# Kernel tuning notes

Hardware: AMD Instinct MI355X
Metric: run time of the kernel (lower is better)

The kernel has to match this reference:

```python
import jax, jax.numpy as jnp
import numpy as np

HIDDEN = 1024
NUM_HEADS = 16
HEAD_DIM = HIDDEN // NUM_HEADS  # 64
B, S = 2, 2048


def setup_inputs() -> dict:
    key = jax.random.key(0)
    ks = jax.random.split(key, 10)
    sd = 1.0 / np.sqrt(HIDDEN)
    x = jax.random.normal(ks[0], (B, S, HIDDEN), dtype=jnp.float32)
    # per-head projections stacked over head axis: [H, hidden, head_dim]
    Wq = jax.random.normal(ks[1], (NUM_HEADS, HIDDEN, HEAD_DIM), dtype=jnp.float32) * sd
    Wk = jax.random.normal(ks[2], (NUM_HEADS, HIDDEN, HEAD_DIM), dtype=jnp.float32) * sd
    Wv = jax.random.normal(ks[3], (NUM_HEADS, HIDDEN, HEAD_DIM), dtype=jnp.float32) * sd
    bq = jax.random.normal(ks[4], (NUM_HEADS, HEAD_DIM), dtype=jnp.float32) * sd
    bk = jax.random.normal(ks[5], (NUM_HEADS, HEAD_DIM), dtype=jnp.float32) * sd
    bv = jax.random.normal(ks[6], (NUM_HEADS, HEAD_DIM), dtype=jnp.float32) * sd
    # output projection: [all_head_size, hidden]
    Wo = jax.random.normal(ks[7], (HIDDEN, HIDDEN), dtype=jnp.float32) * sd
    bo = jax.random.normal(ks[8], (HIDDEN,), dtype=jnp.float32) * sd
    return {"x": x, "Wq": Wq, "bq": bq, "Wk": Wk, "bk": bk,
            "Wv": Wv, "bv": bv, "Wo": Wo, "bo": bo}


def reference(x, Wq, bq, Wk, bk, Wv, bv, Wo, bo):
    # Fused-across-heads equivalent of the per-head Python loop.
    # q,k,v: [B, H, S, Dh]
    q = jnp.einsum('bsd,hde->bhse', x, Wq) + bq[None, :, None, :]
    k = jnp.einsum('bsd,hde->bhse', x, Wk) + bk[None, :, None, :]
    v = jnp.einsum('bsd,hde->bhse', x, Wv) + bv[None, :, None, :]
    scale = 1.0 / jnp.sqrt(jnp.asarray(HEAD_DIM, dtype=x.dtype))
    scores = jnp.einsum('bhse,bhte->bhst', q, k) * scale  # [B,H,S,S]
    probs = jax.nn.softmax(scores, axis=-1)               # dropout=0 (eval)
    ctx = jnp.einsum('bhst,bhte->bhse', probs, v)         # [B,H,S,Dh]
    # concat heads on last dim (head order matches torch.cat over heads)
    ctx = jnp.transpose(ctx, (0, 2, 1, 3)).reshape(x.shape[0], x.shape[1], -1)
    out = ctx @ Wo + bo                                   # output projection
    return out
```

## Files before the change

### kernel.cpp

```cpp
#include <hip/hip_runtime.h>
#include <cstdint>

typedef unsigned short u16;
typedef __attribute__((ext_vector_type(8))) short short8;
typedef __attribute__((ext_vector_type(4))) short short4v;
typedef __attribute__((ext_vector_type(4))) float f32x4;
typedef __attribute__((ext_vector_type(4))) unsigned short u16x4;

__device__ __forceinline__ u16 f2bf(float x) {
    unsigned int u = __float_as_uint(x);
    u += 0x7fffu + ((u >> 16) & 1u);
    return (u16)(u >> 16);
}

__device__ __forceinline__ float fexp2(float x) {
#if __has_builtin(__builtin_amdgcn_exp2f)
    return __builtin_amdgcn_exp2f(x);
#else
    return exp2f(x);
#endif
}

__device__ __forceinline__ unsigned pack_bf16(float a, float b) {
    unsigned ua = __float_as_uint(a) + 0x8000u;
    unsigned ub = __float_as_uint(b) + 0x8000u;
    return __builtin_amdgcn_perm(ub, ua, 0x07060302u);
}

#if __has_builtin(__builtin_amdgcn_mfma_f32_16x16x16bf16_1k)
__device__ __forceinline__ f32x4 mfma16(short4v a, short4v b, f32x4 c) {
    return __builtin_amdgcn_mfma_f32_16x16x16bf16_1k(a, b, c, 0, 0, 0);
}
#else
__device__ __forceinline__ f32x4 mfma16(short4v a, short4v b, f32x4 c) {
    short8 a8 = {a[0], a[1], a[2], a[3], 0, 0, 0, 0};
    short8 b8 = {b[0], b[1], b[2], b[3], 0, 0, 0, 0};
    return __builtin_amdgcn_mfma_f32_16x16x32_bf16(a8, b8, c, 0, 0, 0);
}
#endif

__device__ __forceinline__ void gload_lds16(const u16* g, u16* l) {
    __builtin_amdgcn_global_load_lds(
        (const __attribute__((address_space(1))) void*)(g),
        (__attribute__((address_space(3))) void*)(l),
        16, 0, 0);
}

__global__ __launch_bounds__(256) void cast_x_kernel(const float* __restrict__ x,
                                                     u16* __restrict__ xb) {
    int i = (blockIdx.x * 256 + threadIdx.x) * 4;
    float4 v = *(const float4*)(x + i);
    u16x4 o;
    o.x = f2bf(v.x); o.y = f2bf(v.y); o.z = f2bf(v.z); o.w = f2bf(v.w);
    *(u16x4*)(xb + i) = o;
}

__global__ __launch_bounds__(256) void transpose_cast_kernel(const float* __restrict__ src,
                                                             u16* __restrict__ dst,
                                                             int R, int C) {
    __shared__ u16 tile[64][65];
    const int rb = blockIdx.x * 64, cb = blockIdx.y * 64;
    const size_t matoff = (size_t)blockIdx.z * R * C;
    src += matoff; dst += matoff;
    const int tc = threadIdx.x & 63, tr = threadIdx.x >> 6;
    #pragma unroll
    for (int i = 0; i < 64; i += 4)
        tile[tr + i][tc] = f2bf(src[(size_t)(rb + tr + i) * C + (cb + tc)]);
    __syncthreads();
    #pragma unroll
    for (int i = 0; i < 64; i += 4)
        dst[(size_t)(cb + tr + i) * R + (rb + tc)] = tile[tc][tr + i];
}

__global__ __launch_bounds__(256) void gemm_qkv_kernel(
    const u16* __restrict__ X, const u16* __restrict__ W,
    const float* __restrict__ bq, const float* __restrict__ bk,
    const float* __restrict__ bv,
    u16* __restrict__ qo, u16* __restrict__ ko, u16* __restrict__ vto)
{
    __shared__ __align__(16) u16 As[128 * 32];
    __shared__ __align__(16) u16 Bs[128 * 32];
    const int tid = threadIdx.x;
    const int lane = tid & 63;
    const int wv = tid >> 6;
    const int wm = wv & 1, wn = wv >> 1;
    const int m0 = blockIdx.x * 128;
    const int n0 = blockIdx.y * 128;
    const int c = lane & 15, qd = lane >> 4;

    f32x4 acc[4][4];
    #pragma unroll
    for (int a = 0; a < 4; ++a)
        #pragma unroll
        for (int b2 = 0; b2 < 4; ++b2) acc[a][b2] = f32x4{0.f, 0.f, 0.f, 0.f};

    const u16* Xb = X + (size_t)m0 * 1024;
    const u16* Wb = W + (size_t)n0 * 1024;

    for (int kt = 0; kt < 1024; kt += 32) {
        #pragma unroll
        for (int i = 0; i < 2; ++i) {
            int slot = i * 256 + tid;
            int row = slot >> 2, part = slot & 3;
            gload_lds16(Xb + (size_t)row * 1024 + kt + part * 8, &As[slot * 8]);
            gload_lds16(Wb + (size_t)row * 1024 + kt + part * 8, &Bs[slot * 8]);
        }
        __syncthreads();
        short8 af[4], bf[4];
        #pragma unroll
        for (int mt = 0; mt < 4; ++mt)
            af[mt] = *(const short8*)&As[(wm * 64 + mt * 16 + c) * 32 + qd * 8];
        #pragma unroll
        for (int nt = 0; nt < 4; ++nt)
            bf[nt] = *(const short8*)&Bs[(wn * 64 + nt * 16 + c) * 32 + qd * 8];
        #pragma unroll
        for (int mt = 0; mt < 4; ++mt)
            #pragma unroll
            for (int nt = 0; nt < 4; ++nt)
                acc[mt][nt] = __builtin_amdgcn_mfma_f32_16x16x32_bf16(af[mt], bf[nt], acc[mt][nt], 0, 0, 0);
        __syncthreads();
    }

    #pragma unroll
    for (int mt = 0; mt < 4; ++mt) {
        const int mbase = m0 + wm * 64 + mt * 16 + qd * 4;
        const int b = mbase >> 11;
        #pragma unroll
        for (int nt = 0; nt < 4; ++nt) {
            const int n = n0 + wn * 64 + nt * 16 + c;
            const int mat = n >> 10;
            const int idx = n & 1023;
            const int h = idx >> 6, e = idx & 63;
            const float bias = (mat == 0 ? bq : (mat == 1 ? bk : bv))[idx];
            if (mat == 2) {
                const int s = mbase & 2047;
                u16x4 pv;
                pv.x = f2bf(acc[mt][nt][0] + bias);
                pv.y = f2bf(acc[mt][nt][1] + bias);
                pv.z = f2bf(acc[mt][nt][2] + bias);
                pv.w = f2bf(acc[mt][nt][3] + bias);
                *(u16x4*)(vto + ((((size_t)(b * 16 + h) * 128 + (s >> 4)) * 64 + e) * 16
                                 + (s & 15))) = pv;
            } else {
                const float scale = (mat == 0) ? 0.18033688011112042f : 1.0f;
                u16* dst = (mat == 0) ? qo : ko;
                #pragma unroll
                for (int r = 0; r < 4; ++r) {
                    const int s = (mbase + r) & 2047;
                    dst[((size_t)((b * 16 + h) * 2048 + s)) * 64 + e] =
                        f2bf((acc[mt][nt][r] + bias) * scale);
                }
            }
        }
    }
}

__global__ __launch_bounds__(256) void flash_kernel(
    const u16* __restrict__ Q,
    const u16* __restrict__ K,
    const u16* __restrict__ V2,
    u16* __restrict__ ctx)
{
    __shared__ __align__(16) char pool[34816];
    u16* stage = (u16*)pool;
    float (*Os)[64][66] = (float (*)[64][66])pool;
    float (*Ls)[64] = (float (*)[64])(pool + 33792);

    const int tid = threadIdx.x, lane = tid & 63, w = tid >> 6;
    const int c = lane & 15, qd = lane >> 4;
    const int bid = blockIdx.x;
    const int r5 = bid & 31;
    const int bh = (r5 & 7) * 4 + (r5 >> 3);
    const int q0 = (bid >> 5) * 64;
    const int b = bh >> 4, h = bh & 15;
    const u16* Qh = Q + (size_t)bh * 2048 * 64;
    const u16* Kh = K + (size_t)bh * 2048 * 64;
    const u16* Vh = V2 + (size_t)bh * 128 * 1024;

    u16* Kst = stage + w * 4096;
    u16* Vst = Kst + 2048;

    const int krow8 = lane >> 3;
    const int kgc = (lane & 7) ^ (krow8 & 7);

    short8 qf[4][2];
    #pragma unroll
    for (int qb = 0; qb < 4; ++qb)
        #pragma unroll
        for (int kb = 0; kb < 2; ++kb)
            qf[qb][kb] = *(const short8*)&Qh[(size_t)(q0 + qb * 16 + c) * 64 + kb * 32 + qd * 8];

    f32x4 o[4][4];
    f32x4 ol[4];
    #pragma unroll
    for (int mt = 0; mt < 4; ++mt)
        #pragma unroll
        for (int qb = 0; qb < 4; ++qb) o[mt][qb] = f32x4{0.f, 0.f, 0.f, 0.f};
    #pragma unroll
    for (int qb = 0; qb < 4; ++qb) ol[qb] = f32x4{0.f, 0.f, 0.f, 0.f};
    const short4v ones = {(short)0x3F80, (short)0x3F80, (short)0x3F80, (short)0x3F80};

    {
        const int t0 = w * 512;
        #pragma unroll
        for (int j = 0; j < 2; ++j) {
            const int row = j * 8 + krow8;
            gload_lds16(Kh + (size_t)(t0 + row) * 64 + kgc * 8, Kst + j * 512 + lane * 8);
            gload_lds16(Vh + (size_t)(w * 32) * 1024 + (j * 64 + lane) * 8,
                        Vst + j * 512 + lane * 8);
        }
    }

    for (int it = 0; it < 32; ++it) {
        const int buf = it & 1;
        u16* Kb = Kst + buf * 1024;
        u16* Vb = Vst + buf * 1024;

        __builtin_amdgcn_s_waitcnt(0);
        __builtin_amdgcn_sched_barrier(0);

        short8 kf[2];
        #pragma unroll
        for (int kb = 0; kb < 2; ++kb)
            kf[kb] = *(const short8*)&Kb[c * 64 + ((4 * kb + qd) ^ (c & 7)) * 8];
        short4v vf[4];
        #pragma unroll
        for (int mt = 0; mt < 4; ++mt)
            vf[mt] = *(const short4v*)&Vb[(mt * 16 + c) * 16 + qd * 4];

        __builtin_amdgcn_sched_barrier(0);

        if (it < 31) {
            const int t0n = w * 512 + (it + 1) * 16;
            u16* Kn = Kst + (buf ^ 1) * 1024;
            u16* Vn = Vst + (buf ^ 1) * 1024;
            #pragma unroll
            for (int j = 0; j < 2; ++j) {
                const int row = j * 8 + krow8;
                gload_lds16(Kh + (size_t)(t0n + row) * 64 + kgc * 8, Kn + j * 512 + lane * 8);
                gload_lds16(Vh + (size_t)(t0n >> 4) * 1024 + (j * 64 + lane) * 8,
                            Vn + j * 512 + lane * 8);
            }
        }

        f32x4 sc[4];
        #pragma unroll
        for (int qb = 0; qb < 4; ++qb) {
            sc[qb] = f32x4{0.f, 0.f, 0.f, 0.f};
            sc[qb] = __builtin_amdgcn_mfma_f32_16x16x32_bf16(kf[0], qf[qb][0], sc[qb], 0, 0, 0);
            sc[qb] = __builtin_amdgcn_mfma_f32_16x16x32_bf16(kf[1], qf[qb][1], sc[qb], 0, 0, 0);
        }

        short4v pb[4];
        #pragma unroll
        for (int qb = 0; qb < 4; ++qb) {
            float p0 = fexp2(sc[qb][0]);
            float p1 = fexp2(sc[qb][1]);
            float p2 = fexp2(sc[qb][2]);
            float p3 = fexp2(sc[qb][3]);
            unsigned d0 = pack_bf16(p0, p1);
            unsigned d1 = pack_bf16(p2, p3);
            union { unsigned u[2]; short4v s; } pu;
            pu.u[0] = d0; pu.u[1] = d1;
            pb[qb] = pu.s;
        }

        #pragma unroll
        for (int qb = 0; qb < 4; ++qb) {
            #pragma unroll
            for (int mt = 0; mt < 4; ++mt)
                o[mt][qb] = mfma16(vf[mt], pb[qb], o[mt][qb]);
            ol[qb] = mfma16(ones, pb[qb], ol[qb]);
        }
    }

    __syncthreads();
    if (qd == 0) {
        #pragma unroll
        for (int qb = 0; qb < 4; ++qb) Ls[w][qb * 16 + c] = ol[qb][0];
    }

    if (w >= 2) {
        float (*S)[66] = Os[w - 2];
        #pragma unroll
        for (int mt = 0; mt < 4; ++mt)
            #pragma unroll
            for (int qb = 0; qb < 4; ++qb)
                #pragma unroll
                for (int r = 0; r < 4; ++r)
                    S[mt * 16 + qd * 4 + r][qb * 16 + c] = o[mt][qb][r];
    }
    __syncthreads();
    if (w < 2) {
        float (*S)[66] = Os[w];
        #pragma unroll
        for (int mt = 0; mt < 4; ++mt)
            #pragma unroll
            for (int qb = 0; qb < 4; ++qb)
                #pragma unroll
                for (int r = 0; r < 4; ++r)
                    o[mt][qb][r] += S[mt * 16 + qd * 4 + r][qb * 16 + c];
    }
    __syncthreads();
    if (w == 1) {
        float (*S)[66] = Os[0];
        #pragma unroll
        for (int mt = 0; mt < 4; ++mt)
            #pragma unroll
            for (int qb = 0; qb < 4; ++qb)
                #pragma unroll
                for (int r = 0; r < 4; ++r)
                    S[mt * 16 + qd * 4 + r][qb * 16 + c] = o[mt][qb][r];
    }
    __syncthreads();
    if (w == 0) {
        float (*S)[66] = Os[0];
        float inv[4];
        #pragma unroll
        for (int qb = 0; qb < 4; ++qb) {
            int q = qb * 16 + c;
            float l = (Ls[0][q] + Ls[1][q]) + (Ls[2][q] + Ls[3][q]);
            inv[qb] = __builtin_amdgcn_rcpf(l);
        }
        #pragma unroll
        for (int mt = 0; mt < 4; ++mt)
            #pragma unroll
            for (int qb = 0; qb < 4; ++qb) {
                u16x4 ov;
                #pragma unroll
                for (int r = 0; r < 4; ++r) {
                    float v = (o[mt][qb][r] + S[mt * 16 + qd * 4 + r][qb * 16 + c]) * inv[qb];
                    ((u16*)&ov)[r] = f2bf(v);
                }
                *(u16x4*)&ctx[((size_t)(b * 2048 + q0 + qb * 16 + c)) * 1024
                              + h * 64 + mt * 16 + qd * 4] = ov;
            }
    }
}

__global__ __launch_bounds__(256) void gemm_out_kernel(
    const u16* __restrict__ A, const u16* __restrict__ Wt,
    const float* __restrict__ bo, float* __restrict__ out)
{
    __shared__ __align__(16) u16 As[64 * 32];
    __shared__ __align__(16) u16 Bs[128 * 32];
    const int tid = threadIdx.x;
    const int lane = tid & 63;
    const int wv = tid >> 6;
    const int wm = wv & 1, wn = wv >> 1;
    const int m0 = blockIdx.x * 64;
    const int n0 = blockIdx.y * 128;
    const int c = lane & 15, qd = lane >> 4;

    f32x4 acc[2][4];
    #pragma unroll
    for (int a = 0; a < 2; ++a)
        #pragma unroll
        for (int b2 = 0; b2 < 4; ++b2) acc[a][b2] = f32x4{0.f, 0.f, 0.f, 0.f};

    const u16* Ab = A + (size_t)m0 * 1024;
    const u16* Wb = Wt + (size_t)n0 * 1024;

    for (int kt = 0; kt < 1024; kt += 32) {
        {
            int row = tid >> 2, part = tid & 3;
            gload_lds16(Ab + (size_t)row * 1024 + kt + part * 8, &As[tid * 8]);
        }
        #pragma unroll
        for (int i = 0; i < 2; ++i) {
            int slot = i * 256 + tid;
            int row = slot >> 2, part = slot & 3;
            gload_lds16(Wb + (size_t)row * 1024 + kt + part * 8, &Bs[slot * 8]);
        }
        __syncthreads();
        short8 af[2], bf[4];
        #pragma unroll
        for (int mt = 0; mt < 2; ++mt)
            af[mt] = *(const short8*)&As[(wm * 32 + mt * 16 + c) * 32 + qd * 8];
        #pragma unroll
        for (int nt = 0; nt < 4; ++nt)
            bf[nt] = *(const short8*)&Bs[(wn * 64 + nt * 16 + c) * 32 + qd * 8];
        #pragma unroll
        for (int mt = 0; mt < 2; ++mt)
            #pragma unroll
            for (int nt = 0; nt < 4; ++nt)
                acc[mt][nt] = __builtin_amdgcn_mfma_f32_16x16x32_bf16(af[mt], bf[nt], acc[mt][nt], 0, 0, 0);
        __syncthreads();
    }

    #pragma unroll
    for (int mt = 0; mt < 2; ++mt) {
        const int mbase = m0 + wm * 32 + mt * 16 + qd * 4;
        #pragma unroll
        for (int nt = 0; nt < 4; ++nt) {
            const int n = n0 + wn * 64 + nt * 16 + c;
            const float bias = bo[n];
            #pragma unroll
            for (int r = 0; r < 4; ++r)
                out[(size_t)(mbase + r) * 1024 + n] = acc[mt][nt][r] + bias;
        }
    }
}

extern "C" void kernel_launch(void* const* d_in, const int* in_sizes, int n_in,
                              void* d_out, int out_size, void* d_ws, size_t ws_size,
                              hipStream_t stream) {
    const float* x  = (const float*)d_in[0];
    const float* Wq = (const float*)d_in[1];
    const float* bq = (const float*)d_in[2];
    const float* Wk = (const float*)d_in[3];
    const float* bk = (const float*)d_in[4];
    const float* Wv = (const float*)d_in[5];
    const float* bv = (const float*)d_in[6];
    const float* Wo = (const float*)d_in[7];
    const float* bo = (const float*)d_in[8];
    float* out = (float*)d_out;

    u16* ws    = (u16*)d_ws;
    u16* xb    = ws;
    u16* wqkv  = xb + 4096 * 1024;
    u16* wot   = wqkv + 3072 * 1024;
    u16* qws   = wot + 1024 * 1024;
    u16* kws   = qws + 4194304;
    u16* v2ws  = kws + 4194304;
    u16* ctxws = v2ws + 4194304;

    cast_x_kernel<<<4096, 256, 0, stream>>>(x, xb);
    transpose_cast_kernel<<<dim3(16, 1, 16), 256, 0, stream>>>(Wq, wqkv, 1024, 64);
    transpose_cast_kernel<<<dim3(16, 1, 16), 256, 0, stream>>>(Wk, wqkv + 1024 * 1024, 1024, 64);
    transpose_cast_kernel<<<dim3(16, 1, 16), 256, 0, stream>>>(Wv, wqkv + 2 * 1024 * 1024, 1024, 64);
    transpose_cast_kernel<<<dim3(16, 16, 1), 256, 0, stream>>>(Wo, wot, 1024, 1024);
    gemm_qkv_kernel<<<dim3(32, 24), 256, 0, stream>>>(xb, wqkv, bq, bk, bv, qws, kws, v2ws);
    flash_kernel<<<1024, 256, 0, stream>>>(qws, kws, v2ws, ctxws);
    gemm_out_kernel<<<dim3(64, 8), 256, 0, stream>>>(ctxws, wot, bo, out);
}
```

Baseline: 229.7 us.

## Triple-buffer flash K/V staging and merge prep cast kernels into one launch

The flash attention kernel's per-wave K/V LDS staging grows from double to triple buffering. Loads are now issued two iterations ahead, and a partial vmcnt wait replaces the full waitcnt(0), so global-to-LDS loads overlap more compute. LDS use rises to 48KB and launch bounds now request 3 blocks per CU, which may limit occupancy. Separately, the x cast and the four weight transpose-cast launches are merged into one prep kernel to cut launch overhead. The final iterations issue wrapped-around dummy prefetches, which are drained before the epilogue.

```diff
diff --git a/kernel.cpp b/kernel.cpp
--- a/kernel.cpp
+++ b/kernel.cpp
@@ -46,23 +46,44 @@
         16, 0, 0);
 }
 
-__global__ __launch_bounds__(256) void cast_x_kernel(const float* __restrict__ x,
-                                                     u16* __restrict__ xb) {
-    int i = (blockIdx.x * 256 + threadIdx.x) * 4;
-    float4 v = *(const float4*)(x + i);
-    u16x4 o;
-    o.x = f2bf(v.x); o.y = f2bf(v.y); o.z = f2bf(v.z); o.w = f2bf(v.w);
-    *(u16x4*)(xb + i) = o;
-}
-
-__global__ __launch_bounds__(256) void transpose_cast_kernel(const float* __restrict__ src,
-                                                             u16* __restrict__ dst,
-                                                             int R, int C) {
+__global__ __launch_bounds__(256) void prep_kernel(
+    const float* __restrict__ x,
+    const float* __restrict__ Wq, const float* __restrict__ Wk,
+    const float* __restrict__ Wv, const float* __restrict__ Wo,
+    u16* __restrict__ xb, u16* __restrict__ wqkv, u16* __restrict__ wot)
+{
     __shared__ u16 tile[64][65];
-    const int rb = blockIdx.x * 64, cb = blockIdx.y * 64;
-    const size_t matoff = (size_t)blockIdx.z * R * C;
-    src += matoff; dst += matoff;
+    const int z = blockIdx.z;
     const int tc = threadIdx.x & 63, tr = threadIdx.x >> 6;
+
+    if (z == 1) {
+        const int blk = blockIdx.y * 16 + blockIdx.x;
+        const int base = (blk * 256 + threadIdx.x) * 4;
+        #pragma unroll
+        for (int i = 0; i < 16; ++i) {
+            const int idx = base + i * 262144;
+            float4 v = *(const float4*)(x + idx);
+            u16x4 o;
+            o.x = f2bf(v.x); o.y = f2bf(v.y); o.z = f2bf(v.z); o.w = f2bf(v.w);
+            *(u16x4*)(xb + idx) = o;
+        }
+        return;
+    }
+
+    const float* src;
+    u16* dst;
+    int C, R, rb, cb;
+    if (z == 0) {
+        src = Wo; dst = wot; C = 1024; R = 1024;
+        rb = blockIdx.x * 64; cb = blockIdx.y * 64;
+    } else {
+        const float* W = (z == 2) ? Wq : (z == 3) ? Wk : Wv;
+        const int head = blockIdx.y;
+        src = W + head * 65536;
+        dst = wqkv + (size_t)(z - 2) * 1048576 + head * 65536;
+        C = 64; R = 1024;
+        rb = blockIdx.x * 64; cb = 0;
+    }
     #pragma unroll
     for (int i = 0; i < 64; i += 4)
         tile[tr + i][tc] = f2bf(src[(size_t)(rb + tr + i) * C + (cb + tc)]);
@@ -155,13 +176,13 @@
     }
 }
 
-__global__ __launch_bounds__(256) void flash_kernel(
+__global__ __launch_bounds__(256, 3) void flash_kernel(
     const u16* __restrict__ Q,
     const u16* __restrict__ K,
     const u16* __restrict__ V2,
     u16* __restrict__ ctx)
 {
-    __shared__ __align__(16) char pool[34816];
+    __shared__ __align__(16) char pool[49152];
     u16* stage = (u16*)pool;
     float (*Os)[64][66] = (float (*)[64][66])pool;
     float (*Ls)[64] = (float (*)[64])(pool + 33792);
@@ -177,8 +198,8 @@
     const u16* Kh = K + (size_t)bh * 2048 * 64;
     const u16* Vh = V2 + (size_t)bh * 128 * 1024;
 
-    u16* Kst = stage + w * 4096;
-    u16* Vst = Kst + 2048;
+    u16* Kst = stage + w * 6144;
+    u16* Vst = Kst + 3072;
 
     const int krow8 = lane >> 3;
     const int kgc = (lane & 7) ^ (krow8 & 7);
@@ -200,23 +221,25 @@
     for (int qb = 0; qb < 4; ++qb) ol[qb] = f32x4{0.f, 0.f, 0.f, 0.f};
     const short4v ones = {(short)0x3F80, (short)0x3F80, (short)0x3F80, (short)0x3F80};
 
-    {
-        const int t0 = w * 512;
+    #pragma unroll
+    for (int pit = 0; pit < 2; ++pit) {
+        const int t0 = w * 512 + pit * 16;
         #pragma unroll
         for (int j = 0; j < 2; ++j) {
             const int row = j * 8 + krow8;
-            gload_lds16(Kh + (size_t)(t0 + row) * 64 + kgc * 8, Kst + j * 512 + lane * 8);
-            gload_lds16(Vh + (size_t)(w * 32) * 1024 + (j * 64 + lane) * 8,
-                        Vst + j * 512 + lane * 8);
-        }
-    }
-
+            gload_lds16(Kh + (size_t)(t0 + row) * 64 + kgc * 8,
+                        Kst + pit * 1024 + j * 512 + lane * 8);
+            gload_lds16(Vh + (size_t)(t0 >> 4) * 1024 + (j * 64 + lane) * 8,
+                        Vst + pit * 1024 + j * 512 + lane * 8);
+        }
+    }
+
+    int cur = 0;
     for (int it = 0; it < 32; ++it) {
-        const int buf = it & 1;
-        u16* Kb = Kst + buf * 1024;
-        u16* Vb = Vst + buf * 1024;
-
-        __builtin_amdgcn_s_waitcnt(0);
+        u16* Kb = Kst + cur * 1024;
+        u16* Vb = Vst + cur * 1024;
+
+        __builtin_amdgcn_s_waitcnt(0xF74);
         __builtin_amdgcn_sched_barrier(0);
 
         short8 kf[2];
@@ -230,14 +253,17 @@
 
         __builtin_amdgcn_sched_barrier(0);
 
-        if (it < 31) {
-            const int t0n = w * 512 + (it + 1) * 16;
-            u16* Kn = Kst + (buf ^ 1) * 1024;
-            u16* Vn = Vst + (buf ^ 1) * 1024;
+        {
+            const int itn = (it + 2) & 31;
+            const int t0n = w * 512 + itn * 16;
+            const int nslot = (cur >= 1) ? cur - 1 : 2;
+            u16* Kn = Kst + nslot * 1024;
+            u16* Vn = Vst + nslot * 1024;
             #pragma unroll
             for (int j = 0; j < 2; ++j) {
                 const int row = j * 8 + krow8;
-                gload_lds16(Kh + (size_t)(t0n + row) * 64 + kgc * 8, Kn + j * 512 + lane * 8);
+                gload_lds16(Kh + (size_t)(t0n + row) * 64 + kgc * 8,
+                            Kn + j * 512 + lane * 8);
                 gload_lds16(Vh + (size_t)(t0n >> 4) * 1024 + (j * 64 + lane) * 8,
                             Vn + j * 512 + lane * 8);
             }
@@ -272,8 +298,11 @@
                 o[mt][qb] = mfma16(vf[mt], pb[qb], o[mt][qb]);
             ol[qb] = mfma16(ones, pb[qb], ol[qb]);
         }
-    }
-
+
+        cur = (cur == 2) ? 0 : cur + 1;
+    }
+
+    __builtin_amdgcn_s_waitcnt(0xF70);
     __syncthreads();
     if (qd == 0) {
         #pragma unroll
@@ -425,11 +454,7 @@
     u16* v2ws  = kws + 4194304;
     u16* ctxws = v2ws + 4194304;
 
-    cast_x_kernel<<<4096, 256, 0, stream>>>(x, xb);
-    transpose_cast_kernel<<<dim3(16, 1, 16), 256, 0, stream>>>(Wq, wqkv, 1024, 64);
-    transpose_cast_kernel<<<dim3(16, 1, 16), 256, 0, stream>>>(Wk, wqkv + 1024 * 1024, 1024, 64);
-    transpose_cast_kernel<<<dim3(16, 1, 16), 256, 0, stream>>>(Wv, wqkv + 2 * 1024 * 1024, 1024, 64);
-    transpose_cast_kernel<<<dim3(16, 16, 1), 256, 0, stream>>>(Wo, wot, 1024, 1024);
+    prep_kernel<<<dim3(16, 16, 5), 256, 0, stream>>>(x, Wq, Wk, Wv, Wo, xb, wqkv, wot);
     gemm_qkv_kernel<<<dim3(32, 24), 256, 0, stream>>>(xb, wqkv, bq, bk, bv, qws, kws, v2ws);
     flash_kernel<<<1024, 256, 0, stream>>>(qws, kws, v2ws, ctxws);
     gemm_out_kernel<<<dim3(64, 8), 256, 0, stream>>>(ctxws, wot, bo, out);
```

Result: faster. 200.7 us (-12.6%).
